# Optimization experiments

Measured on AMD Instinct MI355X. Metric: run time of the kernel, lower is better.

Reference implementation:

```python
import jax, jax.numpy as jnp
import numpy as np

N, F, K = 256, 32, 8
B = 65536


def setup_inputs() -> dict:
    key = jax.random.key(0)
    k1, k2, k3, k4 = jax.random.split(key, 4)
    x = jax.random.normal(k1, (B, N), dtype=jnp.float32)
    w_lin = jax.random.normal(k2, (N,), dtype=jnp.float32)
    b_lin = jax.random.normal(k3, (1,), dtype=jnp.float32)
    v = jax.random.normal(k4, (N, F, K), dtype=jnp.float32)
    # feature -> field mapping, matching feature2fielddict = {i: i % F}
    field_idx = jnp.arange(N, dtype=jnp.int32) % F
    return {"x": x, "w_lin": w_lin, "b_lin": b_lin, "v": v, "field_idx": field_idx}


def reference(x, w_lin, b_lin, v, field_idx):
    # linear part: nn.Linear(n, 1)
    linear_part = x @ w_lin[:, None] + b_lin  # [B, 1]
    # A[i, j] = v[i, field[j]]  -> [n, n, k]
    A = v[:, field_idx, :]
    # Wmat[i, j] = <v[i, field[j]], v[j, field[i]]>
    Wmat = jnp.einsum('ijk,jik->ij', A, A)  # [n, n]
    # only strict upper triangle (i < j) contributes
    Wu = jnp.triu(Wmat, k=1)
    # sum_{i<j} Wmat[i,j] * x[:,i] * x[:,j]
    interaction = jnp.einsum('bi,ij,bj->b', x, Wu, x)[:, None]  # [B, 1]
    return linear_part + interaction
```

## Files before the change

### kernel.cpp

```cpp
#include <hip/hip_runtime.h>
#include <hip/hip_bf16.h>


#define FK 256

typedef __attribute__((ext_vector_type(8))) short bf16x8;
typedef __attribute__((ext_vector_type(4))) float f32x4v;

__device__ __forceinline__ unsigned short f2bf(float x) {
    return __builtin_bit_cast(unsigned short, __float2bfloat16(x));
}
__device__ __forceinline__ float bf2f(unsigned short h) {
    return __builtin_bit_cast(float, (unsigned int)h << 16);
}

template<int CTRL>
__device__ __forceinline__ float dppadd(float v) {
    int t = __builtin_amdgcn_update_dpp(0, __builtin_bit_cast(int, v),
                                        CTRL, 0xf, 0xf, true);
    return v + __builtin_bit_cast(float, t);
}

__device__ __forceinline__ void block_sync_novm() {
    asm volatile("s_waitcnt lgkmcnt(0)\n\ts_barrier" ::: "memory");
}

__global__ __launch_bounds__(128) void k_build_m(
    const float* __restrict__ v, const int* __restrict__ fidx,
    unsigned int* __restrict__ mp)
{
    __shared__ int fsh[256];
    int tid = threadIdx.x;
    fsh[tid] = fidx[tid];
    fsh[tid + 128] = fidx[tid + 128];
    __syncthreads();

    int u = blockIdx.x * 128 + tid;
    int f  = u >> 2;
    int l  = f & 63;
    int ct = (f >> 6) & 15;
    int s  = f >> 10;
    int c  = ct * 16 + (l & 15);
    int i80 = (u & 3) * 2;
    int k0 = s * 32 + ((l >> 4) & 3) * 8 + i80;
    int fc = fsh[c];
    unsigned short hh[2];
#pragma unroll
    for (int i = 0; i < 2; ++i) {
        int k = k0 + i;
        float acc = 0.f;
        if (k != c) {
            int fk = fsh[k];
            const float* va = v + k * FK + fc * 8;
            const float* vb = v + c * FK + fk * 8;
#pragma unroll
            for (int j = 0; j < 8; ++j) acc += va[j] * vb[j];
            acc *= 0.5f;
        }
        hh[i] = f2bf(acc);
    }
    mp[u] = (unsigned int)hh[0] | ((unsigned int)hh[1] << 16);
}


struct SmemT {
    unsigned short xs[2][4096];
    float part[2][8][16];
};

__device__ __forceinline__ void stage_write(unsigned short* buf, float4 val,
                                            int row, int chunk) {
    unsigned long long h0 = f2bf(val.x), h1 = f2bf(val.y),
                       h2 = f2bf(val.z), h3 = f2bf(val.w);
    unsigned long long pk = h0 | (h1 << 16) | (h2 << 32) | (h3 << 48);
    int byteoff = row * 512 + ((chunk * 8) ^ ((row & 7) << 4));
    *(unsigned long long*)((char*)buf + byteoff) = pk;
}

__global__ __launch_bounds__(512, 2) void k_main(
    const float* __restrict__ x, const float* __restrict__ w_lin,
    const float* __restrict__ b_lin, const uint4* __restrict__ mpack,
    float* __restrict__ out)
{
    __shared__ SmemT sm;

    const int tid = threadIdx.x;
    const int w   = tid >> 6;
    const int l   = tid & 63;
    const int l15 = l & 15;
    const int lg  = l >> 4;

    const long rowbase = (long)blockIdx.x * 128;
    const float* xg = x + rowbase * 256;

    const int srow = w * 2 + (l >> 5);
    const int sc0  = l & 31;
    const int sc1  = sc0 + 32;

    float4 a0 = *(const float4*)(xg + srow * 256 + sc0 * 4);
    float4 b0 = *(const float4*)(xg + srow * 256 + sc1 * 4);

    bf16x8 Brg[8][2];
#pragma unroll
    for (int s = 0; s < 8; ++s)
#pragma unroll
        for (int ct = 0; ct < 2; ++ct)
            Brg[s][ct] = __builtin_bit_cast(bf16x8,
                mpack[(s * 16 + w * 2 + ct) * 64 + l]);

    const float w0 = w_lin[(w * 2 + 0) * 16 + l15];
    const float w1 = w_lin[(w * 2 + 1) * 16 + l15];
    const float bv = b_lin[0];

    stage_write(sm.xs[0], a0, srow, sc0);
    stage_write(sm.xs[0], b0, srow, sc1);
    float4 pa = *(const float4*)(xg + (16 + srow) * 256 + sc0 * 4);
    float4 pb = *(const float4*)(xg + (16 + srow) * 256 + sc1 * 4);
    block_sync_novm();

    for (int t = 0; t < 8; ++t) {
        const char* xsb = (const char*)sm.xs[t & 1];

        f32x4v acc0 = {w0, w0, w0, w0};
        f32x4v acc1 = {w1, w1, w1, w1};
#pragma unroll
        for (int s = 0; s < 8; ++s) {
            int aoff = l15 * 512 + ((s * 64 + lg * 16) ^ ((l15 & 7) << 4));
            bf16x8 af = *(const bf16x8*)(xsb + aoff);
            acc0 = __builtin_amdgcn_mfma_f32_16x16x32_bf16(af, Brg[s][0], acc0, 0, 0, 0);
            acc1 = __builtin_amdgcn_mfma_f32_16x16x32_bf16(af, Brg[s][1], acc1, 0, 0, 0);
        }

#pragma unroll
        for (int r = 0; r < 4; ++r) {
            int row = lg * 4 + r;
            int sw  = (row & 7) << 4;
            int c0  = (w * 2 + 0) * 16 + l15;
            int c1  = (w * 2 + 1) * 16 + l15;
            unsigned short h0 = *(const unsigned short*)(xsb + row * 512 + ((c0 * 2) ^ sw));
            unsigned short h1 = *(const unsigned short*)(xsb + row * 512 + ((c1 * 2) ^ sw));
            float pp = bf2f(h0) * acc0[r] + bf2f(h1) * acc1[r];
            pp = dppadd<0x121>(pp); pp = dppadd<0x122>(pp);
            pp = dppadd<0x124>(pp); pp = dppadd<0x128>(pp);
            if (l15 == 0) sm.part[t & 1][w][row] = pp;
        }

        if (t < 7) {
            unsigned short* nb = sm.xs[(t + 1) & 1];
            stage_write(nb, pa, srow, sc0);
            stage_write(nb, pb, srow, sc1);
        }
        if (t < 6) {
            pa = *(const float4*)(xg + ((t + 2) * 16 + srow) * 256 + sc0 * 4);
            pb = *(const float4*)(xg + ((t + 2) * 16 + srow) * 256 + sc1 * 4);
        }
        block_sync_novm();

        if (tid < 16) {
            const float (*pt)[16] = sm.part[t & 1];
            float y = pt[0][tid] + pt[1][tid] + pt[2][tid] + pt[3][tid] +
                      pt[4][tid] + pt[5][tid] + pt[6][tid] + pt[7][tid];
            out[rowbase + t * 16 + tid] = y + bv;
        }
    }
}

extern "C" void kernel_launch(void* const* d_in, const int* in_sizes, int n_in,
                              void* d_out, int out_size, void* d_ws, size_t ws_size,
                              hipStream_t stream) {
    const float* x     = (const float*)d_in[0];
    const float* w_lin = (const float*)d_in[1];
    const float* b_lin = (const float*)d_in[2];
    const float* v     = (const float*)d_in[3];
    const int*   fidx  = (const int*)d_in[4];
    float* out = (float*)d_out;
    void* mpack = d_ws;

    k_build_m<<<256, 128, 0, stream>>>(v, fidx, (unsigned int*)mpack);
    k_main<<<512, 512, 0, stream>>>(x, w_lin, b_lin, (const uint4*)mpack, out);
}
```

Baseline: 23.52 us.

## Halve waves per block, give each wave four column tiles of M

The main kernel now runs 4 waves per block instead of 8. Each wave keeps four 16-column tiles of the bf16 interaction matrix in registers and issues four MFMAs per A fragment, so each LDS read of x feeds twice as many MFMAs. Staging is reorganised so each lane loads four float4s per tile and writes them with a new swizzle pattern, and the cross-wave partial reduction shrinks to four entries. This cuts LDS traffic and barrier participants but doubles B-fragment registers per lane, which may hurt occupancy, and halves the number of threads issuing global loads.

```diff
diff --git a/kernel.cpp b/kernel.cpp
--- a/kernel.cpp
+++ b/kernel.cpp
@@ -63,26 +63,28 @@
 }
 
 
-struct SmemT {
-    unsigned short xs[2][4096];
-    float part[2][8][16];
-};
-
-__device__ __forceinline__ void stage_write(unsigned short* buf, float4 val,
-                                            int row, int chunk) {
-    unsigned long long h0 = f2bf(val.x), h1 = f2bf(val.y),
-                       h2 = f2bf(val.z), h3 = f2bf(val.w);
-    unsigned long long pk = h0 | (h1 << 16) | (h2 << 32) | (h3 << 48);
-    int byteoff = row * 512 + ((chunk * 8) ^ ((row & 7) << 4));
-    *(unsigned long long*)((char*)buf + byteoff) = pk;
+__device__ __forceinline__ void stage_tile(unsigned short* buf,
+                                           const float4* pre,
+                                           int row, int l15) {
+    char* b = (char*)buf;
+#pragma unroll
+    for (int j = 0; j < 4; ++j) {
+        unsigned long long h0 = f2bf(pre[j].x), h1 = f2bf(pre[j].y),
+                           h2 = f2bf(pre[j].z), h3 = f2bf(pre[j].w);
+        unsigned long long pk = h0 | (h1 << 16) | (h2 << 32) | (h3 << 48);
+        int chunkB = (l15 >> 1) + 8 * j;
+        int off = row * 512 + ((chunkB ^ (row & 7)) << 4) + (l15 & 1) * 8;
+        *(unsigned long long*)(b + off) = pk;
+    }
 }
 
-__global__ __launch_bounds__(512, 2) void k_main(
+__global__ __launch_bounds__(256, 2) void k_main(
     const float* __restrict__ x, const float* __restrict__ w_lin,
     const float* __restrict__ b_lin, const uint4* __restrict__ mpack,
     float* __restrict__ out)
 {
-    __shared__ SmemT sm;
+    __shared__ unsigned short xs[2][4096];
+    __shared__ float part[2][4][16];
 
     const int tid = threadIdx.x;
     const int w   = tid >> 6;
@@ -93,73 +95,78 @@
     const long rowbase = (long)blockIdx.x * 128;
     const float* xg = x + rowbase * 256;
 
-    const int srow = w * 2 + (l >> 5);
-    const int sc0  = l & 31;
-    const int sc1  = sc0 + 32;
+    const int srow = w * 4 + lg;
 
-    float4 a0 = *(const float4*)(xg + srow * 256 + sc0 * 4);
-    float4 b0 = *(const float4*)(xg + srow * 256 + sc1 * 4);
+    float4 pre[4];
+#pragma unroll
+    for (int j = 0; j < 4; ++j)
+        pre[j] = *(const float4*)(xg + srow * 256 + (l15 + 16 * j) * 4);
 
-    bf16x8 Brg[8][2];
+    bf16x8 Brg[8][4];
 #pragma unroll
     for (int s = 0; s < 8; ++s)
 #pragma unroll
-        for (int ct = 0; ct < 2; ++ct)
-            Brg[s][ct] = __builtin_bit_cast(bf16x8,
-                mpack[(s * 16 + w * 2 + ct) * 64 + l]);
+        for (int c = 0; c < 4; ++c)
+            Brg[s][c] = __builtin_bit_cast(bf16x8,
+                mpack[(s * 16 + w * 4 + c) * 64 + l]);
 
-    const float w0 = w_lin[(w * 2 + 0) * 16 + l15];
-    const float w1 = w_lin[(w * 2 + 1) * 16 + l15];
+    float wv4[4];
+#pragma unroll
+    for (int c = 0; c < 4; ++c)
+        wv4[c] = w_lin[(w * 4 + c) * 16 + l15];
     const float bv = b_lin[0];
 
-    stage_write(sm.xs[0], a0, srow, sc0);
-    stage_write(sm.xs[0], b0, srow, sc1);
-    float4 pa = *(const float4*)(xg + (16 + srow) * 256 + sc0 * 4);
-    float4 pb = *(const float4*)(xg + (16 + srow) * 256 + sc1 * 4);
+    stage_tile(xs[0], pre, srow, l15);
+#pragma unroll
+    for (int j = 0; j < 4; ++j)
+        pre[j] = *(const float4*)(xg + (16 + srow) * 256 + (l15 + 16 * j) * 4);
     block_sync_novm();
 
     for (int t = 0; t < 8; ++t) {
-        const char* xsb = (const char*)sm.xs[t & 1];
+        const char* xsb = (const char*)xs[t & 1];
 
-        f32x4v acc0 = {w0, w0, w0, w0};
-        f32x4v acc1 = {w1, w1, w1, w1};
+        f32x4v acc[4];
+#pragma unroll
+        for (int c = 0; c < 4; ++c)
+            acc[c] = f32x4v{wv4[c], wv4[c], wv4[c], wv4[c]};
 #pragma unroll
         for (int s = 0; s < 8; ++s) {
             int aoff = l15 * 512 + ((s * 64 + lg * 16) ^ ((l15 & 7) << 4));
             bf16x8 af = *(const bf16x8*)(xsb + aoff);
-            acc0 = __builtin_amdgcn_mfma_f32_16x16x32_bf16(af, Brg[s][0], acc0, 0, 0, 0);
-            acc1 = __builtin_amdgcn_mfma_f32_16x16x32_bf16(af, Brg[s][1], acc1, 0, 0, 0);
+            acc[0] = __builtin_amdgcn_mfma_f32_16x16x32_bf16(af, Brg[s][0], acc[0], 0, 0, 0);
+            acc[1] = __builtin_amdgcn_mfma_f32_16x16x32_bf16(af, Brg[s][1], acc[1], 0, 0, 0);
+            acc[2] = __builtin_amdgcn_mfma_f32_16x16x32_bf16(af, Brg[s][2], acc[2], 0, 0, 0);
+            acc[3] = __builtin_amdgcn_mfma_f32_16x16x32_bf16(af, Brg[s][3], acc[3], 0, 0, 0);
         }
 
 #pragma unroll
         for (int r = 0; r < 4; ++r) {
             int row = lg * 4 + r;
             int sw  = (row & 7) << 4;
-            int c0  = (w * 2 + 0) * 16 + l15;
-            int c1  = (w * 2 + 1) * 16 + l15;
-            unsigned short h0 = *(const unsigned short*)(xsb + row * 512 + ((c0 * 2) ^ sw));
-            unsigned short h1 = *(const unsigned short*)(xsb + row * 512 + ((c1 * 2) ^ sw));
-            float pp = bf2f(h0) * acc0[r] + bf2f(h1) * acc1[r];
+            float pp = 0.f;
+#pragma unroll
+            for (int c = 0; c < 4; ++c) {
+                int col = (w * 4 + c) * 16 + l15;
+                unsigned short h = *(const unsigned short*)(xsb + row * 512 + ((col * 2) ^ sw));
+                pp += bf2f(h) * acc[c][r];
+            }
             pp = dppadd<0x121>(pp); pp = dppadd<0x122>(pp);
             pp = dppadd<0x124>(pp); pp = dppadd<0x128>(pp);
-            if (l15 == 0) sm.part[t & 1][w][row] = pp;
+            if (l15 == 0) part[t & 1][w][row] = pp;
         }
 
-        if (t < 7) {
-            unsigned short* nb = sm.xs[(t + 1) & 1];
-            stage_write(nb, pa, srow, sc0);
-            stage_write(nb, pb, srow, sc1);
-        }
+        if (t < 7)
+            stage_tile(xs[(t + 1) & 1], pre, srow, l15);
         if (t < 6) {
-            pa = *(const float4*)(xg + ((t + 2) * 16 + srow) * 256 + sc0 * 4);
-            pb = *(const float4*)(xg + ((t + 2) * 16 + srow) * 256 + sc1 * 4);
+#pragma unroll
+            for (int j = 0; j < 4; ++j)
+                pre[j] = *(const float4*)(xg + ((t + 2) * 16 + srow) * 256 + (l15 + 16 * j) * 4);
         }
         block_sync_novm();
 
         if (tid < 16) {
-            const float (*pt)[16] = sm.part[t & 1];
-            float y = pt[0][tid] + pt[1][tid] + pt[2][tid] + pt[3][tid] +
-                      pt[4][tid] + pt[5][tid] + pt[6][tid] + pt[7][tid];
+            float y = part[t & 1][0][tid] + part[t & 1][1][tid] +
+                      part[t & 1][2][tid] + part[t & 1][3][tid];
             out[rowbase + t * 16 + tid] = y + bv;
         }
     }
@@ -177,5 +184,5 @@
     void* mpack = d_ws;
 
     k_build_m<<<256, 128, 0, stream>>>(v, fidx, (unsigned int*)mpack);
-    k_main<<<512, 512, 0, stream>>>(x, w_lin, b_lin, (const uint4*)mpack, out);
+    k_main<<<512, 256, 0, stream>>>(x, w_lin, b_lin, (const uint4*)mpack, out);
 }
```

Result: no change. 23.73 us (+0.9%).
